# Performance work log

Measured on AMD Instinct MI355X. Metric: run time of the kernel, lower is better.

Reference implementation:

```python
import jax, jax.numpy as jnp
import numpy as np

N_NODES = 15000
N_EDGES = 30000
NUM_GRAPHS = 600
N_STEMS = 6000
N_JBONDS = 3000
DIM = 64
NUM_FEAT = 14
NUM_OUT_PER_STEM = 105


def _lin(a, w, b):
    return a @ w.T + b


def _forward(x, edge_attr, lin0_w, lin0_b, en1_w, en1_b, en2_w, en2_b, root_w, conv_b,
             gru_w_ih, gru_w_hh, gru_b_ih, gru_b_hh, s1_w, s1_b, s2_w, s2_b,
             j1_w, j1_b, j2_w, j2_b, lstm_w_ih, lstm_w_hh, lstm_b_ih, lstm_b_hh,
             lout_w, lout_b, edge_index, stem_atmidx, jbond_atmidx, batch):
    n, dim = x.shape[0], lin0_w.shape[0]
    lrelu = jax.nn.leaky_relu  # negative_slope=0.01 as in torch default
    src, dst = edge_index[0], edge_index[1]

    out = lrelu(_lin(x, lin0_w, lin0_b))
    h = out  # GRU hidden state [N, dim]

    # Edge-conditioned weights (NNConv): small MLP on edge_attr -> [E, dim, dim]
    We = _lin(lrelu(_lin(edge_attr, en1_w, en1_b)), en2_w, en2_b).reshape(-1, dim, dim)
    deg = jnp.clip(jax.ops.segment_sum(jnp.ones_like(dst, dtype=x.dtype), dst, num_segments=n), 1.0)

    for _ in range(6):
        # gather source features, per-edge matvec, scatter-mean to destinations
        msg = jnp.einsum('ei,eio->eo', out[src], We)
        agg = jax.ops.segment_sum(msg, dst, num_segments=n) / deg[:, None]
        m = lrelu(agg + out @ root_w + conv_b)
        # GRUCell (torch gate order: r, z, n)
        gi = _lin(m, gru_w_ih, gru_b_ih)
        gh = _lin(h, gru_w_hh, gru_b_hh)
        ir, iz, inn = jnp.split(gi, 3, axis=-1)
        hr, hz, hn = jnp.split(gh, 3, axis=-1)
        r = jax.nn.sigmoid(ir + hr)
        z = jax.nn.sigmoid(iz + hz)
        ng = jnp.tanh(inn + r * hn)
        h = (1.0 - z) * ng + z * h
        out = h

    stem_preds = _lin(lrelu(_lin(out[stem_atmidx], s1_w, s1_b)), s2_w, s2_b)
    jb = _lin(lrelu(_lin(out[jbond_atmidx.reshape(-1)], j1_w, j1_b)), j2_w, j2_b)
    jbond_preds = jb.reshape(jbond_atmidx.shape).mean(axis=1)

    # Set2Set with 1 processing step (LSTM input 2*dim -> hidden dim)
    b = NUM_GRAPHS
    q_star = jnp.zeros((b, 2 * dim), x.dtype)
    hl = jnp.zeros((b, dim), x.dtype)
    cl = jnp.zeros((b, dim), x.dtype)
    gates = _lin(q_star, lstm_w_ih, lstm_b_ih) + _lin(hl, lstm_w_hh, lstm_b_hh)
    i_, f_, g_, o_ = jnp.split(gates, 4, axis=-1)  # torch LSTM gate order i,f,g,o
    c = jax.nn.sigmoid(f_) * cl + jax.nn.sigmoid(i_) * jnp.tanh(g_)
    q = jax.nn.sigmoid(o_) * jnp.tanh(c)
    e = (out * q[batch]).sum(axis=-1)  # [N]
    emax = jax.ops.segment_max(e, batch, num_segments=b)
    a_un = jnp.exp(e - emax[batch])
    a = a_un / jax.ops.segment_sum(a_un, batch, num_segments=b)[batch]
    r_pool = jax.ops.segment_sum(a[:, None] * out, batch, num_segments=b)
    q_star = jnp.concatenate([q, r_pool], axis=-1)  # [B, 2*dim]

    final = _lin(q_star, lout_w, lout_b)  # [B, 2]
    return final, stem_preds, jbond_preds


def setup_inputs() -> dict:
    key = jax.random.key(0)
    ks = jax.random.split(key, 40)
    d = DIM

    def rn(k, shape, s=0.1):
        return jax.random.normal(k, shape, dtype=jnp.float32) * s

    inp = {}
    inp['x'] = jax.random.normal(ks[0], (N_NODES, NUM_FEAT), dtype=jnp.float32)
    inp['edge_attr'] = jax.random.uniform(ks[1], (N_EDGES, 4), dtype=jnp.float32)
    inp['lin0_w'] = rn(ks[2], (d, NUM_FEAT)); inp['lin0_b'] = rn(ks[3], (d,))
    inp['en1_w'] = rn(ks[4], (d, 4)); inp['en1_b'] = rn(ks[5], (d,))
    inp['en2_w'] = rn(ks[6], (d * d, d), 0.02); inp['en2_b'] = rn(ks[7], (d * d,), 0.02)
    inp['root_w'] = rn(ks[8], (d, d)); inp['conv_b'] = rn(ks[9], (d,))
    inp['gru_w_ih'] = rn(ks[10], (3 * d, d)); inp['gru_w_hh'] = rn(ks[11], (3 * d, d))
    inp['gru_b_ih'] = rn(ks[12], (3 * d,)); inp['gru_b_hh'] = rn(ks[13], (3 * d,))
    inp['s1_w'] = rn(ks[14], (d, d)); inp['s1_b'] = rn(ks[15], (d,))
    inp['s2_w'] = rn(ks[16], (NUM_OUT_PER_STEM, d)); inp['s2_b'] = rn(ks[17], (NUM_OUT_PER_STEM,))
    inp['j1_w'] = rn(ks[18], (d, d)); inp['j1_b'] = rn(ks[19], (d,))
    inp['j2_w'] = rn(ks[20], (1, d)); inp['j2_b'] = rn(ks[21], (1,))
    inp['lstm_w_ih'] = rn(ks[22], (4 * d, 2 * d)); inp['lstm_w_hh'] = rn(ks[23], (4 * d, d))
    inp['lstm_b_ih'] = rn(ks[24], (4 * d,)); inp['lstm_b_hh'] = rn(ks[25], (4 * d,))
    inp['lout_w'] = rn(ks[26], (2, 2 * d)); inp['lout_b'] = rn(ks[27], (2,))
    inp['edge_index'] = jax.random.randint(ks[28], (2, N_EDGES), 0, N_NODES)
    inp['stem_atmidx'] = jax.random.randint(ks[29], (N_STEMS,), 0, N_NODES)
    inp['jbond_atmidx'] = jax.random.randint(ks[30], (N_JBONDS, 2), 0, N_NODES)
    inp['batch'] = jnp.sort(jax.random.randint(ks[31], (N_NODES,), 0, NUM_GRAPHS))
    return inp


def reference(x, edge_attr, lin0_w, lin0_b, en1_w, en1_b, en2_w, en2_b, root_w, conv_b,
              gru_w_ih, gru_w_hh, gru_b_ih, gru_b_hh, s1_w, s1_b, s2_w, s2_b,
              j1_w, j1_b, j2_w, j2_b, lstm_w_ih, lstm_w_hh, lstm_b_ih, lstm_b_hh,
              lout_w, lout_b, edge_index, stem_atmidx, jbond_atmidx, batch):
    return _forward(x, edge_attr, lin0_w, lin0_b, en1_w, en1_b, en2_w, en2_b, root_w, conv_b,
                    gru_w_ih, gru_w_hh, gru_b_ih, gru_b_hh, s1_w, s1_b, s2_w, s2_b,
                    j1_w, j1_b, j2_w, j2_b, lstm_w_ih, lstm_w_hh, lstm_b_ih, lstm_b_hh,
                    lout_w, lout_b, edge_index, stem_atmidx, jbond_atmidx, batch)
```

## Files before the change

kernel.cpp:

```cpp
#include <hip/hip_runtime.h>

typedef unsigned short u16;
typedef unsigned int   u32;

#define N_NODES    15000
#define PADN       15008
#define N_EDGES    30000
#define NUM_GRAPHS 600
#define N_STEMS    6000
#define N_JBONDS   3000

#define OUT_FINAL  0
#define OUT_STEM   1200
#define OUT_JB     631200

#define A1S 68
#define N_CVT 26

#define EBLK 32
#define EGRIDE 938
#define KCH 130
#define A1LS 66
#define RS   66

#define NGROUPS (PADN/16)
#define NWTILES 28
#define HS 72

#define PACK_W2B_N (KCH*2048)
#define PACK_NW_N  (NWTILES*4*512)
#define PACK_HD_N  1792
#define PACK_TOTAL (PACK_W2B_N + PACK_NW_N + PACK_HD_N)

typedef short frag8 __attribute__((ext_vector_type(8)));
typedef float facc4 __attribute__((ext_vector_type(4)));
typedef _Float16 h16x2 __attribute__((ext_vector_type(2)));

__device__ __forceinline__ float u2f(u16 v){ union{u32 i; float f;} c; c.i=((u32)v)<<16; return c.f; }
__device__ __forceinline__ u16  f2b(float f){ union{float f; u32 u;} c; c.f=f; u32 u=c.u;
                                              return (u16)((u + 0x7fffu + ((u>>16)&1u))>>16); }
__device__ __forceinline__ u16  f2h(float f){ union{_Float16 h; u16 u;} c; c.h = (_Float16)f; return c.u; }
__device__ __forceinline__ float h2f(u16 v){ union{u16 u; _Float16 h;} c; c.u = v; return (float)c.h; }
__device__ __forceinline__ float lrelu(float x){ return x>0.f ? x : 0.01f*x; }
__device__ __forceinline__ float sigmoidf(float x){ return 1.f/(1.f+expf(-x)); }

__device__ __forceinline__ int lower_bound_i(const int* __restrict__ a, int n, int v){
  int lo=0, hi=n;
  while(lo<hi){ int m=(lo+hi)>>1; if(a[m]<v) lo=m+1; else hi=m; }
  return lo;
}

__device__ __forceinline__ void store_out(void* dout, int isf, int idx, float v){
  if(isf) ((float*)dout)[idx] = v;
  else    ((u16*)dout)[idx]   = f2b(v);
}

__device__ __forceinline__ frag8 pack4h(uint4 v, u32 av2){
  union { u32 d[4]; frag8 f; } au;
  h16x2 a; { union{u32 u; h16x2 h;} c; c.u = av2; a = c.h; }
  { union{u32 u; h16x2 h;} c; c.u = v.x; c.h = a * c.h; au.d[0] = c.u; }
  { union{u32 u; h16x2 h;} c; c.u = v.y; c.h = a * c.h; au.d[1] = c.u; }
  { union{u32 u; h16x2 h;} c; c.u = v.z; c.h = a * c.h; au.d[2] = c.u; }
  { union{u32 u; h16x2 h;} c; c.u = v.w; c.h = a * c.h; au.d[3] = c.u; }
  return au.f;
}

__global__ __launch_bounds__(256) void k_sniff(const u16* __restrict__ x, int n, int* __restrict__ flag,
                                               float* __restrict__ deg, float* __restrict__ agg,
                                               float* __restrict__ outF, u16* __restrict__ outB){
  int tid = blockIdx.x*256 + threadIdx.x;
  int stride = gridDim.x*256;
  int local = 0;
  for(int i = tid; i < n; i += stride){
    u16 v = x[i];
    if(((v>>7)&0xFFu) == 0xFFu) local = 1;
  }
  if(local) atomicOr(flag, 1);
  float4 z = (float4){0.f,0.f,0.f,0.f};
  for(int i = tid; i < PADN; i += stride) deg[i] = 0.f;
  for(int i = tid; i < PADN*64/4; i += stride) ((float4*)agg)[i] = z;
  for(int i = tid; i < (PADN-N_NODES)*64/4; i += stride) ((float4*)(outF + (size_t)N_NODES*64))[i] = z;
  for(int i = tid; i < (PADN-N_NODES)*64/8; i += stride) ((float4*)(outB + (size_t)N_NODES*64))[i] = z;
}

struct CvtArgs { const void* src[N_CVT]; float* dst[N_CVT]; int n[N_CVT]; };

__global__ __launch_bounds__(256) void k_cvt(CvtArgs A, const int* __restrict__ flag){
  int isf = *flag;
  int tid = blockIdx.x*256 + threadIdx.x;
  int stride = gridDim.x*256;
  for(int b=0; b<N_CVT; b++){
    int n = A.n[b];
    const float* sf = (const float*)A.src[b];
    const u16*   sb = (const u16*)A.src[b];
    float* d = A.dst[b];
    for(int i=tid; i<n; i+=stride) d[i] = isf ? sf[i] : u2f(sb[i]);
  }
}

__global__ __launch_bounds__(64) void k_lin0(const float* __restrict__ x, const float* __restrict__ w,
                                             const float* __restrict__ b,
                                             float* __restrict__ outF, u16* __restrict__ outB){
  int n = blockIdx.x, o = threadIdx.x;
  __shared__ float xs[14];
  if(o<14) xs[o] = x[n*14+o];
  __syncthreads();
  float acc = b[o];
  #pragma unroll
  for(int i=0;i<14;i++) acc += xs[i]*w[o*14+i];
  float v = lrelu(acc);
  outF[n*64+o] = v;
  outB[n*64+o] = f2h(v);
}

__global__ __launch_bounds__(128) void k_a1(const float* __restrict__ ea,
                                            const float* __restrict__ en1w, const float* __restrict__ en1b,
                                            u16* __restrict__ a1b,
                                            const int* __restrict__ ei, float* __restrict__ deg){
  int e = blockIdx.x, k = threadIdx.x;
  if(k >= A1S) return;
  float v = 0.f;
  if(k < 64){
    float acc = en1b[k];
    #pragma unroll
    for(int c=0;c<4;c++) acc += ea[e*4+c] * en1w[k*4+c];
    v = lrelu(acc);
  } else if(k == 64) v = 1.0f;
  a1b[e*A1S + k] = f2h(v);
  if(k == 65) atomicAdd(&deg[ei[N_EDGES + e]], 1.0f);
}

__global__ __launch_bounds__(256) void k_packAll(const float* __restrict__ en2w, const float* __restrict__ en2b,
                                                 u16* __restrict__ B2b,
                                                 const float* __restrict__ rootw, const float* __restrict__ wih,
                                                 const float* __restrict__ whh, u16* __restrict__ gBn,
                                                 const float* __restrict__ s1w, const float* __restrict__ s2w,
                                                 const float* __restrict__ j1w,
                                                 float4* __restrict__ s1P, float4* __restrict__ s2P,
                                                 float4* __restrict__ j1P){
  int idx = blockIdx.x*256 + threadIdx.x;
  if(idx < PACK_W2B_N){
    int jj  = idx & 7;
    int l   = (idx >> 3) & 63;
    int nt  = (idx >> 9) & 3;
    int c   = idx >> 11;
    int q = l >> 4, m16 = l & 15;
    int kidx = c*32 + q*8 + jj;
    int k = kidx >> 6, j = kidx & 63;
    int o = nt*16 + m16;
    float v = (k < 64) ? en2w[((size_t)(j*64 + o))*64 + k] : en2b[j*64 + o];
    B2b[idx] = f2h(v);
    return;
  }
  idx -= PACK_W2B_N;
  if(idx < PACK_NW_N){
    int jj = idx & 7, l = (idx>>3) & 63, ch = (idx>>9) & 3, t = idx >> 11;
    int m16 = l & 15, q = l >> 4;
    int j = ((ch & 1) ? 32 : 0) + q*8 + jj;
    float v;
    if(t < 4){        int o = t*16 + m16;        v = rootw[j*64 + o]; }
    else if(t < 16){  int g = (t-4)*16 + m16;    v = wih[(size_t)g*64 + j]; }
    else {            int g = (t-16)*16 + m16;   v = whh[(size_t)g*64 + j]; }
    u16 hb = f2h(v);
    gBn[idx] = (ch >> 1) ? f2h(v - h2f(hb)) : hb;
    return;
  }
  idx -= PACK_NW_N;
  if(idx < PACK_HD_N){
    if(idx < 1024){
      int o = idx & 63, j4 = idx >> 6;
      const float* r = s1w + o*64 + 4*j4;
      s1P[idx] = (float4){r[0], r[1], r[2], r[3]};
      const float* r2 = j1w + o*64 + 4*j4;
      j1P[idx] = (float4){r2[0], r2[1], r2[2], r2[3]};
    }
    {
      int j4 = idx / 112, t = idx % 112;
      float4 v = {0.f,0.f,0.f,0.f};
      if(t < 105){
        const float* r = s2w + t*64 + 4*j4;
        v = (float4){r[0], r[1], r[2], r[3]};
      }
      s2P[idx] = v;
    }
  }
}

__global__ __launch_bounds__(512, 4) void k_egemm(const u16* __restrict__ outB,
                                               const u16* __restrict__ a1b,
                                               const u16* __restrict__ B2b,
                                               const int* __restrict__ ei,
                                               float* __restrict__ agg){
  int tid = threadIdx.x;
  int l = tid & 63, w = tid >> 6;
  int m16 = l & 15, q = l >> 4;
  int eb = blockIdx.x * EBLK;

  __shared__ __align__(16) u16 a1l[EBLK*A1LS];
  __shared__ __align__(16) float red[4][EBLK*RS];

  int e0 = eb + m16, e1 = eb + 16 + m16;
  int n0 = (e0 < N_EDGES) ? ei[e0] : 0;
  int n1 = (e1 < N_EDGES) ? ei[e1] : 0;
  uint4 o200 = *(const uint4*)(outB + (size_t)n0*64 +      q*8);
  uint4 o201 = *(const uint4*)(outB + (size_t)n0*64 + 32 + q*8);
  uint4 o210 = *(const uint4*)(outB + (size_t)n1*64 +      q*8);
  uint4 o211 = *(const uint4*)(outB + (size_t)n1*64 + 32 + q*8);

  for(int idx = tid; idx < EBLK*33; idx += 512){
    int r = idx / 33, c = idx - r*33;
    int e = eb + r;
    u32 v = (e < N_EDGES) ? ((const u32*)(a1b + (size_t)e*A1S))[c] : 0u;
    ((u32*)a1l)[r*33 + c] = v;
  }
  __syncthreads();

  facc4 acc[2][4];
  #pragma unroll
  for(int t=0;t<2;t++)
    #pragma unroll
    for(int nt=0;nt<4;nt++) acc[t][nt] = (facc4){0.f,0.f,0.f,0.f};

  int ks = (w*65) >> 3, ke = ((w+1)*65) >> 3;
  const frag8* __restrict__ Bg = (const frag8*)B2b;

  frag8 bA[4], bB[4];
  #pragma unroll
  for(int nt=0;nt<4;nt++) bA[nt] = Bg[(size_t)(2*ks)*256 + nt*64 + l];

  for(int k = ks; k < ke; ++k){
    #pragma unroll
    for(int nt=0;nt<4;nt++) bB[nt] = Bg[(size_t)(2*k+1)*256 + nt*64 + l];

    u32 a0 = a1l[m16*A1LS + k];
    u32 a1v = a1l[(16+m16)*A1LS + k];
    u32 av0 = a0 | (a0 << 16);
    u32 av1 = a1v | (a1v << 16);

    {
      frag8 au0 = pack4h(o200, av0);
      frag8 au1 = pack4h(o210, av1);
      #pragma unroll
      for(int nt=0;nt<4;nt++)
        acc[0][nt] = __builtin_amdgcn_mfma_f32_16x16x32_f16(au0, bA[nt], acc[0][nt], 0,0,0);
      #pragma unroll
      for(int nt=0;nt<4;nt++)
        acc[1][nt] = __builtin_amdgcn_mfma_f32_16x16x32_f16(au1, bA[nt], acc[1][nt], 0,0,0);
    }

    int kn = (k+1 < ke) ? (k+1) : k;
    #pragma unroll
    for(int nt=0;nt<4;nt++) bA[nt] = Bg[(size_t)(2*kn)*256 + nt*64 + l];

    {
      frag8 au0 = pack4h(o201, av0);
      frag8 au1 = pack4h(o211, av1);
      #pragma unroll
      for(int nt=0;nt<4;nt++)
        acc[0][nt] = __builtin_amdgcn_mfma_f32_16x16x32_f16(au0, bB[nt], acc[0][nt], 0,0,0);
      #pragma unroll
      for(int nt=0;nt<4;nt++)
        acc[1][nt] = __builtin_amdgcn_mfma_f32_16x16x32_f16(au1, bB[nt], acc[1][nt], 0,0,0);
    }
  }

  if(w < 4){
    #pragma unroll
    for(int t = 0; t < 2; t++)
      #pragma unroll
      for(int nt = 0; nt < 4; nt++)
        #pragma unroll
        for(int r = 0; r < 4; r++){
          int el = t*16 + q*4 + r;
          red[w][el*RS + nt*16 + m16] = acc[t][nt][r];
        }
  }
  __syncthreads();
  if(w >= 4){
    #pragma unroll
    for(int t = 0; t < 2; t++)
      #pragma unroll
      for(int nt = 0; nt < 4; nt++)
        #pragma unroll
        for(int r = 0; r < 4; r++){
          int el = t*16 + q*4 + r;
          red[w-4][el*RS + nt*16 + m16] += acc[t][nt][r];
        }
  }
  __syncthreads();

  for(int i = tid; i < EBLK*64; i += 512){
    int el = i >> 6, o = i & 63;
    int e = eb + el;
    if(e < N_EDGES){
      float s = red[0][el*RS + o] + red[1][el*RS + o]
              + red[2][el*RS + o] + red[3][el*RS + o];
      atomicAdd(&agg[(size_t)ei[N_EDGES + e]*64 + o], s);
    }
  }
}

__global__ __launch_bounds__(256) void k_node(float* __restrict__ agg, const float* __restrict__ deg,
                                              float* __restrict__ outF, u16* __restrict__ outB,
                                              const u16* __restrict__ gBn, const float* __restrict__ convb,
                                              const float* __restrict__ bih, const float* __restrict__ bhh){
  int tid = threadIdx.x;
  int l = tid & 63, w = tid >> 6;
  int m16 = l & 15, q = l >> 4;
  int nb = blockIdx.x * 16;

  __shared__ __align__(16) u16 hhi[16][HS], hlo[16][HS];
  __shared__ __align__(16) u16 mhi[16][HS], mlo[16][HS];

  {
    float4 v = ((const float4*)(outF + (size_t)nb*64))[tid];
    int base = tid*4;
    int node = base >> 6, o = base & 63;
    float vv[4] = {v.x, v.y, v.z, v.w};
    #pragma unroll
    for(int t=0;t<4;t++){
      u16 hb = f2h(vv[t]);
      hhi[node][o+t] = hb;
      hlo[node][o+t] = f2h(vv[t] - h2f(hb));
    }
  }
  __syncthreads();

  const frag8* __restrict__ Bg = (const frag8*)gBn;

#define GEMM6(ACC, A0, A1, L0, L1, T)                                      \
  {                                                                        \
    const frag8* bp = Bg + (size_t)(T)*256 + l;                            \
    frag8 b0 = bp[0], b1 = bp[64], b2 = bp[128], b3 = bp[192];             \
    ACC = __builtin_amdgcn_mfma_f32_16x16x32_f16(A0, b0, ACC, 0,0,0);      \
    ACC = __builtin_amdgcn_mfma_f32_16x16x32_f16(A1, b1, ACC, 0,0,0);      \
    ACC = __builtin_amdgcn_mfma_f32_16x16x32_f16(L0, b0, ACC, 0,0,0);      \
    ACC = __builtin_amdgcn_mfma_f32_16x16x32_f16(L1, b1, ACC, 0,0,0);      \
    ACC = __builtin_amdgcn_mfma_f32_16x16x32_f16(A0, b2, ACC, 0,0,0);      \
    ACC = __builtin_amdgcn_mfma_f32_16x16x32_f16(A1, b3, ACC, 0,0,0);      \
  }

  frag8 hA0 = *(const frag8*)&hhi[m16][q*8];
  frag8 hA1 = *(const frag8*)&hhi[m16][32 + q*8];
  frag8 hL0 = *(const frag8*)&hlo[m16][q*8];
  frag8 hL1 = *(const frag8*)&hlo[m16][32 + q*8];

  facc4 dR  = (facc4){0.f,0.f,0.f,0.f};
  facc4 ghA = (facc4){0.f,0.f,0.f,0.f};
  facc4 ghB = (facc4){0.f,0.f,0.f,0.f};
  facc4 ghC = (facc4){0.f,0.f,0.f,0.f};
  GEMM6(dR,  hA0, hA1, hL0, hL1, w);
  GEMM6(ghA, hA0, hA1, hL0, hL1, 16 + w);
  GEMM6(ghB, hA0, hA1, hL0, hL1, 20 + w);
  GEMM6(ghC, hA0, hA1, hL0, hL1, 24 + w);

  int o = w*16 + m16;
  float cb = convb[o];
  #pragma unroll
  for(int r=0;r<4;r++){
    int node = q*4 + r;
    int n = nb + node;
    float a = agg[(size_t)n*64 + o] / fmaxf(deg[n], 1.0f) + dR[r] + cb;
    agg[(size_t)n*64 + o] = 0.f;
    float mv = lrelu(a);
    u16 mb = f2h(mv);
    mhi[node][o] = mb;
    mlo[node][o] = f2h(mv - h2f(mb));
  }
  __syncthreads();

  frag8 mA0 = *(const frag8*)&mhi[m16][q*8];
  frag8 mA1 = *(const frag8*)&mhi[m16][32 + q*8];
  frag8 mL0 = *(const frag8*)&mlo[m16][q*8];
  frag8 mL1 = *(const frag8*)&mlo[m16][32 + q*8];

  facc4 giA = (facc4){0.f,0.f,0.f,0.f};
  facc4 giB = (facc4){0.f,0.f,0.f,0.f};
  facc4 giC = (facc4){0.f,0.f,0.f,0.f};
  GEMM6(giA, mA0, mA1, mL0, mL1, 4 + w);
  GEMM6(giB, mA0, mA1, mL0, mL1, 8 + w);
  GEMM6(giC, mA0, mA1, mL0, mL1, 12 + w);
#undef GEMM6

  float bi0 = bih[o], bi1 = bih[64+o], bi2 = bih[128+o];
  float bh0 = bhh[o], bh1 = bhh[64+o], bh2 = bhh[128+o];
  #pragma unroll
  for(int r=0;r<4;r++){
    int node = q*4 + r;
    int n = nb + node;
    float ir = giA[r]+bi0, iz = giB[r]+bi1, inn = giC[r]+bi2;
    float hr = ghA[r]+bh0, hz = ghB[r]+bh1, hn = ghC[r]+bh2;
    float rr  = sigmoidf(ir + hr);
    float z   = sigmoidf(iz + hz);
    float ngv = tanhf(inn + rr*hn);
    float hold = h2f(hhi[node][o]) + h2f(hlo[node][o]);
    float hnew = (1.f - z)*ngv + z*hold;
    if(n < N_NODES){
      outF[(size_t)n*64 + o] = hnew;
      outB[(size_t)n*64 + o] = f2h(hnew);
    }
  }
}

__global__ __launch_bounds__(512) void k_stem(const float* __restrict__ outF, const int* __restrict__ sidx,
                                              const float4* __restrict__ s1P, const float* __restrict__ s1b,
                                              const float4* __restrict__ s2P, const float* __restrict__ s2b,
                                              void* __restrict__ dout, const int* __restrict__ flag){
  int grp = threadIdx.x >> 7, t = threadIdx.x & 127;
  int s = blockIdx.x*4 + grp;
  int isf = *flag;
  __shared__ __align__(16) float xs[4][64], hid[4][64];
  int a = sidx[s];
  if(t < 64) xs[grp][t] = outF[(size_t)a*64 + t];
  __syncthreads();
  if(t < 64){
    float acc = s1b[t];
    const float4* xp = (const float4*)xs[grp];
    #pragma unroll 8
    for(int j4=0;j4<16;j4++){
      float4 w = s1P[j4*64+t];
      float4 x = xp[j4];
      acc += w.x*x.x + w.y*x.y + w.z*x.z + w.w*x.w;
    }
    hid[grp][t] = lrelu(acc);
  }
  __syncthreads();
  if(t < 105){
    float acc = s2b[t];
    const float4* hp = (const float4*)hid[grp];
    #pragma unroll 8
    for(int j4=0;j4<16;j4++){
      float4 w = s2P[j4*112+t];
      float4 h = hp[j4];
      acc += w.x*h.x + w.y*h.y + w.z*h.z + w.w*h.w;
    }
    store_out(dout, isf, OUT_STEM + s*105 + t, acc);
  }
}

__global__ __launch_bounds__(512) void k_jbond(const float* __restrict__ outF, const int* __restrict__ jidx,
                                               const float4* __restrict__ j1P, const float* __restrict__ j1b,
                                               const float* __restrict__ j2w, const float* __restrict__ j2b,
                                               void* __restrict__ dout, const int* __restrict__ flag){
  int grp = threadIdx.x >> 7, t = threadIdx.x & 127;
  int jb = blockIdx.x*4 + grp;
  int isf = *flag;
  __shared__ __align__(16) float xs[4][2][64], hid[4][2][64];
  int at = t >> 6, k = t & 63;
  int a = jidx[jb*2 + at];
  xs[grp][at][k] = outF[(size_t)a*64 + k];
  __syncthreads();
  {
    float acc = j1b[k];
    const float4* xp = (const float4*)xs[grp][at];
    #pragma unroll 8
    for(int j4=0;j4<16;j4++){
      float4 w = j1P[j4*64+k];
      float4 x = xp[j4];
      acc += w.x*x.x + w.y*x.y + w.z*x.z + w.w*x.w;
    }
    hid[grp][at][k] = lrelu(acc);
  }
  __syncthreads();
  if(t < 64){
    float p = (hid[grp][0][t] + hid[grp][1][t]) * j2w[t];
    #pragma unroll
    for(int s=32;s;s>>=1) p += __shfl_xor(p, s, 64);
    if(t==0) store_out(dout, isf, OUT_JB + jb, 0.5f*p + j2b[0]);
  }
}

__global__ __launch_bounds__(64) void k_s2s(const float* __restrict__ outF, const int* __restrict__ batch,
                                            const float* __restrict__ bih, const float* __restrict__ bhh,
                                            const float* __restrict__ loutw, const float* __restrict__ loutb,
                                            void* __restrict__ dout, const int* __restrict__ flag){
  int b = blockIdx.x, t = threadIdx.x;
  int isf = *flag;
  float i_ = bih[t]     + bhh[t];
  float g_ = bih[128+t] + bhh[128+t];
  float o_ = bih[192+t] + bhh[192+t];
  float c  = sigmoidf(i_)*tanhf(g_);
  float q  = sigmoidf(o_)*tanhf(c);

  int lo = lower_bound_i(batch, N_NODES, b);
  int hi = lower_bound_i(batch, N_NODES, b+1);

  float emax = -3.4e38f;
  for(int n=lo;n<hi;n++){
    float p = outF[n*64+t]*q;
    #pragma unroll
    for(int s=32;s;s>>=1) p += __shfl_xor(p, s, 64);
    emax = fmaxf(emax, p);
  }
  float Z = 0.f, racc = 0.f;
  for(int n=lo;n<hi;n++){
    float v = outF[n*64+t];
    float p = v*q;
    #pragma unroll
    for(int s=32;s;s>>=1) p += __shfl_xor(p, s, 64);
    float w = expf(p - emax);
    Z += w; racc += w*v;
  }
  float rp = (hi>lo) ? racc/Z : 0.f;

  #pragma unroll
  for(int j=0;j<2;j++){
    float p = q*loutw[j*128+t] + rp*loutw[j*128+64+t];
    #pragma unroll
    for(int s=32;s;s>>=1) p += __shfl_xor(p, s, 64);
    if(t==0) store_out(dout, isf, OUT_FINAL + b*2 + j, p + loutb[j]);
  }
}

extern "C" void kernel_launch(void* const* d_in, const int* in_sizes, int n_in,
                              void* d_out, int out_size, void* d_ws, size_t ws_size,
                              hipStream_t stream) {
  const int* edge_index  = (const int*)d_in[28];
  const int* stem_atmidx = (const int*)d_in[29];
  const int* jbond_atmidx= (const int*)d_in[30];
  const int* batch       = (const int*)d_in[31];

  char* ws = (char*)d_ws;
  size_t off = 0;
  auto alloc = [&](size_t bytes)->void*{ void* p = ws + off; off = (off + bytes + 255) & ~(size_t)255; return p; };

  int*   flag = (int*)  alloc(4);
  float* outF = (float*)alloc((size_t)PADN*64*4);
  u16*   outB = (u16*)  alloc((size_t)PADN*64*2);
  float* agg  = (float*)alloc((size_t)PADN*64*4);
  u16*   a1b  = (u16*)  alloc((size_t)N_EDGES*A1S*2);
  u16*   B2b  = (u16*)  alloc((size_t)KCH*2048*2 + 2048*2);
  u16*   gBn  = (u16*)  alloc((size_t)NWTILES*4*512*2);
  float* deg  = (float*)alloc((size_t)PADN*4);
  float4* s1P   = (float4*)alloc(1024*16);
  float4* s2P   = (float4*)alloc(1792*16);
  float4* j1P   = (float4*)alloc(1024*16);

  static const int cvt_idx[N_CVT] = {0,1,2,3,4,5,6,7,8,9,10,11,12,13,14,15,16,17,18,19,20,21,24,25,26,27};
  CvtArgs A;
  float* cF[N_CVT];
  for(int i=0;i<N_CVT;i++){
    int src = cvt_idx[i];
    int n = in_sizes[src];
    cF[i] = (float*)alloc((size_t)n*4);
    A.src[i] = d_in[src];
    A.dst[i] = cF[i];
    A.n[i]   = n;
  }
  (void)ws_size; (void)n_in; (void)out_size;
  float* xF=cF[0];   float* eaF=cF[1];  float* l0w=cF[2];  float* l0b=cF[3];
  float* e1w=cF[4];  float* e1b=cF[5];  float* e2w=cF[6];  float* e2b=cF[7];
  float* rootw=cF[8];float* convb=cF[9];
  float* wih=cF[10]; float* whh=cF[11]; float* bih=cF[12]; float* bhh=cF[13];
  float* s1w=cF[14]; float* s1b=cF[15]; float* s2w=cF[16]; float* s2b=cF[17];
  float* j1w=cF[18]; float* j1b=cF[19]; float* j2w=cF[20]; float* j2b=cF[21];
  float* lbih=cF[22];float* lbhh=cF[23];float* loutw=cF[24];float* loutb=cF[25];

  hipMemsetAsync(flag, 0, 4, stream);

  k_sniff <<<128, 256, 0, stream>>>((const u16*)d_in[0], in_sizes[0], flag, deg, agg, outF, outB);
  k_cvt   <<<512, 256, 0, stream>>>(A, flag);

  k_lin0    <<<N_NODES, 64, 0, stream>>>(xF, l0w, l0b, outF, outB);
  k_a1      <<<N_EDGES, 128, 0, stream>>>(eaF, e1w, e1b, a1b, edge_index, deg);
  k_packAll <<<PACK_TOTAL/256, 256, 0, stream>>>(e2w, e2b, B2b, rootw, wih, whh, gBn,
                                                 s1w, s2w, j1w, s1P, s2P, j1P);

  for(int it=0; it<6; it++){
    k_egemm<<<EGRIDE, 512, 0, stream>>>(outB, a1b, B2b, edge_index, agg);
    k_node <<<NGROUPS, 256, 0, stream>>>(agg, deg, outF, outB, gBn, convb, bih, bhh);
  }

  k_stem <<<N_STEMS/4, 512, 0, stream>>>(outF, stem_atmidx, s1P, s1b, s2P, s2b, d_out, flag);
  k_jbond<<<N_JBONDS/4, 512, 0, stream>>>(outF, jbond_atmidx, j1P, j1b, j2w, j2b, d_out, flag);
  k_s2s  <<<NUM_GRAPHS, 64, 0, stream>>>(outF, batch, lbih, lbhh, loutw, loutb, d_out, flag);
}
```

Measured before the change: 458.9 us.

## Sort edges by destination and write segment sums without atomics

Builds a destination-sorted edge list once, using a count pass, a single-block prefix scan and a scatter. Each edge-GEMM block then takes the edges between run boundaries near its 32-edge window. It sums each destination's messages in shared memory and stores them straight to agg, replacing the per-element float atomicAdds. A three-tile template handles windows that stretch to as many as 48 edges. In exchange it adds setup kernels, indirect gathers through sidx, lowers the occupancy hint from 4 to 2 blocks and uses more LDS; a destination run longer than the 48-edge cap would be truncated.

```diff
diff --git a/kernel.cpp b/kernel.cpp
--- a/kernel.cpp
+++ b/kernel.cpp
@@ -17,8 +17,8 @@
 #define A1S 68
 #define N_CVT 26
 
-#define EBLK 32
 #define EGRIDE 938
+#define ECAP 48
 #define KCH 130
 #define A1LS 66
 #define RS   66
@@ -67,7 +67,8 @@
 
 __global__ __launch_bounds__(256) void k_sniff(const u16* __restrict__ x, int n, int* __restrict__ flag,
                                                float* __restrict__ deg, float* __restrict__ agg,
-                                               float* __restrict__ outF, u16* __restrict__ outB){
+                                               float* __restrict__ outF, u16* __restrict__ outB,
+                                               int* __restrict__ cnt){
   int tid = blockIdx.x*256 + threadIdx.x;
   int stride = gridDim.x*256;
   int local = 0;
@@ -77,7 +78,7 @@
   }
   if(local) atomicOr(flag, 1);
   float4 z = (float4){0.f,0.f,0.f,0.f};
-  for(int i = tid; i < PADN; i += stride) deg[i] = 0.f;
+  for(int i = tid; i < PADN; i += stride){ deg[i] = 0.f; cnt[i] = 0; }
   for(int i = tid; i < PADN*64/4; i += stride) ((float4*)agg)[i] = z;
   for(int i = tid; i < (PADN-N_NODES)*64/4; i += stride) ((float4*)(outF + (size_t)N_NODES*64))[i] = z;
   for(int i = tid; i < (PADN-N_NODES)*64/8; i += stride) ((float4*)(outB + (size_t)N_NODES*64))[i] = z;
@@ -116,7 +117,8 @@
 __global__ __launch_bounds__(128) void k_a1(const float* __restrict__ ea,
                                             const float* __restrict__ en1w, const float* __restrict__ en1b,
                                             u16* __restrict__ a1b,
-                                            const int* __restrict__ ei, float* __restrict__ deg){
+                                            const int* __restrict__ ei, float* __restrict__ deg,
+                                            int* __restrict__ cnt){
   int e = blockIdx.x, k = threadIdx.x;
   if(k >= A1S) return;
   float v = 0.f;
@@ -128,6 +130,47 @@
   } else if(k == 64) v = 1.0f;
   a1b[e*A1S + k] = f2h(v);
   if(k == 65) atomicAdd(&deg[ei[N_EDGES + e]], 1.0f);
+  if(k == 66) atomicAdd(&cnt[ei[N_EDGES + e]], 1);
+}
+
+__global__ __launch_bounds__(1024) void k_scan(const int* __restrict__ cnt,
+                                               int* __restrict__ startA, int* __restrict__ cursor){
+  __shared__ int part[1024];
+  int th = threadIdx.x;
+  int base = th*15;
+  int loc[15];
+  int s = 0;
+  #pragma unroll
+  for(int i=0;i<15;i++){
+    int idx = base+i;
+    int v = (idx < PADN) ? cnt[idx] : 0;
+    loc[i] = s; s += v;
+  }
+  part[th] = s;
+  __syncthreads();
+  for(int off=1; off<1024; off<<=1){
+    int v = part[th];
+    int u = (th >= off) ? part[th-off] : 0;
+    __syncthreads();
+    part[th] = v + u;
+    __syncthreads();
+  }
+  int pre = (th==0) ? 0 : part[th-1];
+  #pragma unroll
+  for(int i=0;i<15;i++){
+    int idx = base+i;
+    if(idx < PADN){ int v = pre + loc[i]; startA[idx] = v; cursor[idx] = v; }
+  }
+}
+
+__global__ __launch_bounds__(256) void k_scatter(const int* __restrict__ ei, int* __restrict__ cursor,
+                                                 int* __restrict__ sidx, int* __restrict__ sdst){
+  int e = blockIdx.x*256 + threadIdx.x;
+  if(e < N_EDGES){
+    int d = ei[N_EDGES + e];
+    int pos = atomicAdd(&cursor[d], 1);
+    sidx[pos] = e; sdst[pos] = d;
+  }
 }
 
 __global__ __launch_bounds__(256) void k_packAll(const float* __restrict__ en2w, const float* __restrict__ en2b,
@@ -186,116 +229,151 @@
   }
 }
 
-__global__ __launch_bounds__(512, 4) void k_egemm(const u16* __restrict__ outB,
+template<int NT>
+__device__ __forceinline__ void egemm_core(int l, int w, int m16, int q, int n,
+                                           const u16* __restrict__ outB,
+                                           const frag8* __restrict__ Bg,
+                                           const u16* a1l, const int* srcL, float* red){
+  uint4 oE[NT], oO[NT];
+  #pragma unroll
+  for(int t=0;t<NT;t++){
+    int node = srcL[t*16 + m16];
+    oE[t] = *(const uint4*)(outB + (size_t)node*64 +      q*8);
+    oO[t] = *(const uint4*)(outB + (size_t)node*64 + 32 + q*8);
+  }
+
+  facc4 acc[NT][4];
+  #pragma unroll
+  for(int t=0;t<NT;t++)
+    #pragma unroll
+    for(int nt=0;nt<4;nt++) acc[t][nt] = (facc4){0.f,0.f,0.f,0.f};
+
+  int ks = (w*65) >> 3, ke = ((w+1)*65) >> 3;
+
+  frag8 bA[4], bB[4];
+  #pragma unroll
+  for(int nt=0;nt<4;nt++) bA[nt] = Bg[(size_t)(2*ks)*256 + nt*64 + l];
+
+  for(int k = ks; k < ke; ++k){
+    #pragma unroll
+    for(int nt=0;nt<4;nt++) bB[nt] = Bg[(size_t)(2*k+1)*256 + nt*64 + l];
+
+    u32 av[NT];
+    #pragma unroll
+    for(int t=0;t<NT;t++){
+      u32 a = a1l[(t*16 + m16)*A1LS + k];
+      av[t] = a | (a << 16);
+    }
+
+    #pragma unroll
+    for(int t=0;t<NT;t++){
+      frag8 a = pack4h(oE[t], av[t]);
+      #pragma unroll
+      for(int nt=0;nt<4;nt++)
+        acc[t][nt] = __builtin_amdgcn_mfma_f32_16x16x32_f16(a, bA[nt], acc[t][nt], 0,0,0);
+    }
+
+    int kn = (k+1 < ke) ? (k+1) : k;
+    #pragma unroll
+    for(int nt=0;nt<4;nt++) bA[nt] = Bg[(size_t)(2*kn)*256 + nt*64 + l];
+
+    #pragma unroll
+    for(int t=0;t<NT;t++){
+      frag8 a = pack4h(oO[t], av[t]);
+      #pragma unroll
+      for(int nt=0;nt<4;nt++)
+        acc[t][nt] = __builtin_amdgcn_mfma_f32_16x16x32_f16(a, bB[nt], acc[t][nt], 0,0,0);
+    }
+  }
+
+  float* slab = red + (size_t)((w < 4) ? w : (w-4)) * (ECAP*RS);
+  if(w < 4){
+    #pragma unroll
+    for(int t=0;t<NT;t++)
+      #pragma unroll
+      for(int nt=0;nt<4;nt++)
+        #pragma unroll
+        for(int r=0;r<4;r++){
+          int el = t*16 + q*4 + r;
+          slab[el*RS + nt*16 + m16] = acc[t][nt][r];
+        }
+  }
+  __syncthreads();
+  if(w >= 4){
+    #pragma unroll
+    for(int t=0;t<NT;t++)
+      #pragma unroll
+      for(int nt=0;nt<4;nt++)
+        #pragma unroll
+        for(int r=0;r<4;r++){
+          int el = t*16 + q*4 + r;
+          slab[el*RS + nt*16 + m16] += acc[t][nt][r];
+        }
+  }
+  __syncthreads();
+}
+
+__global__ __launch_bounds__(512, 2) void k_egemm(const u16* __restrict__ outB,
                                                const u16* __restrict__ a1b,
                                                const u16* __restrict__ B2b,
                                                const int* __restrict__ ei,
+                                               const int* __restrict__ sidx,
+                                               const int* __restrict__ sdst,
                                                float* __restrict__ agg){
   int tid = threadIdx.x;
   int l = tid & 63, w = tid >> 6;
   int m16 = l & 15, q = l >> 4;
-  int eb = blockIdx.x * EBLK;
-
-  __shared__ __align__(16) u16 a1l[EBLK*A1LS];
-  __shared__ __align__(16) float red[4][EBLK*RS];
-
-  int e0 = eb + m16, e1 = eb + 16 + m16;
-  int n0 = (e0 < N_EDGES) ? ei[e0] : 0;
-  int n1 = (e1 < N_EDGES) ? ei[e1] : 0;
-  uint4 o200 = *(const uint4*)(outB + (size_t)n0*64 +      q*8);
-  uint4 o201 = *(const uint4*)(outB + (size_t)n0*64 + 32 + q*8);
-  uint4 o210 = *(const uint4*)(outB + (size_t)n1*64 +      q*8);
-  uint4 o211 = *(const uint4*)(outB + (size_t)n1*64 + 32 + q*8);
-
-  for(int idx = tid; idx < EBLK*33; idx += 512){
+  int w32 = blockIdx.x * 32;
+
+  __shared__ __align__(16) u16 a1l[ECAP*A1LS];
+  __shared__ __align__(16) float red[4*ECAP*RS];
+  __shared__ int sdstW[52];
+  __shared__ int srcL[ECAP];
+
+  for(int i = tid; i < 52; i += 512){
+    int j = w32 - 1 + i;
+    sdstW[i] = (j < 0) ? -1 : ((j < N_EDGES) ? sdst[j] : -2);
+  }
+  __syncthreads();
+
+  int li = 1;
+  while(li < 52 && sdstW[li] == sdstW[li-1]) li++;
+  int hiI = 33;
+  while(hiI < 52 && sdstW[hiI] == sdstW[hiI-1]) hiI++;
+  int lo = w32 - 1 + li;
+  int hi = w32 - 1 + hiI; if(hi > N_EDGES) hi = N_EDGES;
+  int n = hi - lo; if(n < 0) n = 0; if(n > ECAP) n = ECAP;
+
+  for(int el = tid; el < ECAP; el += 512)
+    srcL[el] = (el < n) ? ei[sidx[lo + el]] : 0;
+  for(int idx = tid; idx < ECAP*33; idx += 512){
     int r = idx / 33, c = idx - r*33;
-    int e = eb + r;
-    u32 v = (e < N_EDGES) ? ((const u32*)(a1b + (size_t)e*A1S))[c] : 0u;
+    u32 v = 0;
+    if(r < n){
+      int orig = sidx[lo + r];
+      v = ((const u32*)(a1b + (size_t)orig*A1S))[c];
+    }
     ((u32*)a1l)[r*33 + c] = v;
   }
   __syncthreads();
 
-  facc4 acc[2][4];
-  #pragma unroll
-  for(int t=0;t<2;t++)
-    #pragma unroll
-    for(int nt=0;nt<4;nt++) acc[t][nt] = (facc4){0.f,0.f,0.f,0.f};
-
-  int ks = (w*65) >> 3, ke = ((w+1)*65) >> 3;
   const frag8* __restrict__ Bg = (const frag8*)B2b;
-
-  frag8 bA[4], bB[4];
-  #pragma unroll
-  for(int nt=0;nt<4;nt++) bA[nt] = Bg[(size_t)(2*ks)*256 + nt*64 + l];
-
-  for(int k = ks; k < ke; ++k){
-    #pragma unroll
-    for(int nt=0;nt<4;nt++) bB[nt] = Bg[(size_t)(2*k+1)*256 + nt*64 + l];
-
-    u32 a0 = a1l[m16*A1LS + k];
-    u32 a1v = a1l[(16+m16)*A1LS + k];
-    u32 av0 = a0 | (a0 << 16);
-    u32 av1 = a1v | (a1v << 16);
-
-    {
-      frag8 au0 = pack4h(o200, av0);
-      frag8 au1 = pack4h(o210, av1);
-      #pragma unroll
-      for(int nt=0;nt<4;nt++)
-        acc[0][nt] = __builtin_amdgcn_mfma_f32_16x16x32_f16(au0, bA[nt], acc[0][nt], 0,0,0);
-      #pragma unroll
-      for(int nt=0;nt<4;nt++)
-        acc[1][nt] = __builtin_amdgcn_mfma_f32_16x16x32_f16(au1, bA[nt], acc[1][nt], 0,0,0);
-    }
-
-    int kn = (k+1 < ke) ? (k+1) : k;
-    #pragma unroll
-    for(int nt=0;nt<4;nt++) bA[nt] = Bg[(size_t)(2*kn)*256 + nt*64 + l];
-
-    {
-      frag8 au0 = pack4h(o201, av0);
-      frag8 au1 = pack4h(o211, av1);
-      #pragma unroll
-      for(int nt=0;nt<4;nt++)
-        acc[0][nt] = __builtin_amdgcn_mfma_f32_16x16x32_f16(au0, bB[nt], acc[0][nt], 0,0,0);
-      #pragma unroll
-      for(int nt=0;nt<4;nt++)
-        acc[1][nt] = __builtin_amdgcn_mfma_f32_16x16x32_f16(au1, bB[nt], acc[1][nt], 0,0,0);
-    }
-  }
-
-  if(w < 4){
-    #pragma unroll
-    for(int t = 0; t < 2; t++)
-      #pragma unroll
-      for(int nt = 0; nt < 4; nt++)
-        #pragma unroll
-        for(int r = 0; r < 4; r++){
-          int el = t*16 + q*4 + r;
-          red[w][el*RS + nt*16 + m16] = acc[t][nt][r];
-        }
-  }
-  __syncthreads();
-  if(w >= 4){
-    #pragma unroll
-    for(int t = 0; t < 2; t++)
-      #pragma unroll
-      for(int nt = 0; nt < 4; nt++)
-        #pragma unroll
-        for(int r = 0; r < 4; r++){
-          int el = t*16 + q*4 + r;
-          red[w-4][el*RS + nt*16 + m16] += acc[t][nt][r];
-        }
-  }
-  __syncthreads();
-
-  for(int i = tid; i < EBLK*64; i += 512){
+  if(n <= 32) egemm_core<2>(l, w, m16, q, n, outB, Bg, a1l, srcL, red);
+  else        egemm_core<3>(l, w, m16, q, n, outB, Bg, a1l, srcL, red);
+
+  for(int i = tid; i < n*64; i += 512){
     int el = i >> 6, o = i & 63;
-    int e = eb + el;
-    if(e < N_EDGES){
-      float s = red[0][el*RS + o] + red[1][el*RS + o]
-              + red[2][el*RS + o] + red[3][el*RS + o];
-      atomicAdd(&agg[(size_t)ei[N_EDGES + e]*64 + o], s);
+    int d = sdstW[li + el];
+    bool first = (el == 0) || (sdstW[li + el - 1] != d);
+    if(first){
+      float s = 0.f;
+      int e2 = el;
+      while(e2 < n && sdstW[li + e2] == d){
+        s += red[0*ECAP*RS + e2*RS + o] + red[1*ECAP*RS + e2*RS + o]
+           + red[2*ECAP*RS + e2*RS + o] + red[3*ECAP*RS + e2*RS + o];
+        e2++;
+      }
+      agg[(size_t)d*64 + o] = s;
     }
   }
 }
@@ -532,6 +610,11 @@
   u16*   B2b  = (u16*)  alloc((size_t)KCH*2048*2 + 2048*2);
   u16*   gBn  = (u16*)  alloc((size_t)NWTILES*4*512*2);
   float* deg  = (float*)alloc((size_t)PADN*4);
+  int*   cnt    = (int*)alloc((size_t)PADN*4);
+  int*   startA = (int*)alloc((size_t)PADN*4);
+  int*   cursor = (int*)alloc((size_t)PADN*4);
+  int*   sidx   = (int*)alloc((size_t)N_EDGES*4);
+  int*   sdst   = (int*)alloc((size_t)N_EDGES*4);
   float4* s1P   = (float4*)alloc(1024*16);
   float4* s2P   = (float4*)alloc(1792*16);
   float4* j1P   = (float4*)alloc(1024*16);
@@ -558,16 +641,18 @@
 
   hipMemsetAsync(flag, 0, 4, stream);
 
-  k_sniff <<<128, 256, 0, stream>>>((const u16*)d_in[0], in_sizes[0], flag, deg, agg, outF, outB);
+  k_sniff <<<128, 256, 0, stream>>>((const u16*)d_in[0], in_sizes[0], flag, deg, agg, outF, outB, cnt);
   k_cvt   <<<512, 256, 0, stream>>>(A, flag);
 
   k_lin0    <<<N_NODES, 64, 0, stream>>>(xF, l0w, l0b, outF, outB);
-  k_a1      <<<N_EDGES, 128, 0, stream>>>(eaF, e1w, e1b, a1b, edge_index, deg);
+  k_a1      <<<N_EDGES, 128, 0, stream>>>(eaF, e1w, e1b, a1b, edge_index, deg, cnt);
   k_packAll <<<PACK_TOTAL/256, 256, 0, stream>>>(e2w, e2b, B2b, rootw, wih, whh, gBn,
                                                  s1w, s2w, j1w, s1P, s2P, j1P);
+  k_scan    <<<1, 1024, 0, stream>>>(cnt, startA, cursor);
+  k_scatter <<<(N_EDGES+255)/256, 256, 0, stream>>>(edge_index, cursor, sidx, sdst);
 
   for(int it=0; it<6; it++){
-    k_egemm<<<EGRIDE, 512, 0, stream>>>(outB, a1b, B2b, edge_index, agg);
+    k_egemm<<<EGRIDE, 512, 0, stream>>>(outB, a1b, B2b, edge_index, sidx, sdst, agg);
     k_node <<<NGROUPS, 256, 0, stream>>>(agg, deg, outF, outB, gBn, convb, bih, bhh);
   }
 
```

Measured after the change: 480.8 us. +4.8%, slower.
